# Kernel tuning notes

Hardware: AMD Instinct MI355X
Metric: run time of the kernel (lower is better)

Reference implementation:

```python
import jax, jax.numpy as jnp
import numpy as np

B, S, M, H, NH, FF = 8, 512, 512, 1024, 16, 4096
DH = H // NH      # 64
K = M + S         # key length = mem_len + sentence_len
EPS = 1e-5


def setup_inputs() -> dict:
    key = jax.random.key(0)
    ks = jax.random.split(key, 14)
    p = lambda k, shp: jax.random.normal(k, shp, jnp.float32) * 0.02
    return {
        "token_embedding": jax.random.normal(ks[0], (B, S, H), jnp.float32),
        "rel_pos_embedding": jax.random.normal(ks[1], (K, H), jnp.float32),
        "mems": jax.random.normal(ks[2], (B, M, H), jnp.float32),
        "segment_num": 1,
        "layer_num": 0,
        "Wq": p(ks[3], (H, H)), "Wk": p(ks[4], (H, H)), "Wv": p(ks[5], (H, H)),
        "Wr": p(ks[6], (H, H)), "Wo": p(ks[7], (H, H)),
        "u_bias": p(ks[8], (NH, DH)), "v_bias": p(ks[9], (NH, DH)),
        "gamma": jnp.ones((H,), jnp.float32), "beta": jnp.zeros((H,), jnp.float32),
        "W1": p(ks[10], (H, FF)), "b1": jnp.zeros((FF,), jnp.float32),
        "W2": p(ks[11], (FF, H)), "b2": jnp.zeros((H,), jnp.float32),
    }


def _rel_shift(x):
    # Transformer-XL relative shift. x: [B, NH, S, K]
    b, nh, s, k = x.shape
    x = jnp.pad(x, ((0, 0), (0, 0), (0, 0), (1, 0)))          # [B,NH,S,K+1]
    x = x.reshape(b, nh, k + 1, s)[:, :, 1:, :]               # drop first row
    return x.reshape(b, nh, s, k)


def _layer_norm(x, gamma, beta):
    mu = jnp.mean(x, axis=-1, keepdims=True)
    var = jnp.mean(jnp.square(x - mu), axis=-1, keepdims=True)
    return (x - mu) / jnp.sqrt(var + EPS) * gamma + beta


def reference(token_embedding, rel_pos_embedding, mems, segment_num, layer_num,
              Wq, Wk, Wv, Wr, Wo, u_bias, v_bias, gamma, beta, W1, b1, W2, b2):
    x = token_embedding                                   # [B,S,H]
    cat = jnp.concatenate([mems, x], axis=1)              # [B,K,H]
    q = (x @ Wq).reshape(B, S, NH, DH)
    k = (cat @ Wk).reshape(B, K, NH, DH)
    v = (cat @ Wv).reshape(B, K, NH, DH)
    r = (rel_pos_embedding @ Wr).reshape(K, NH, DH)
    # content + position terms (Transformer-XL)
    AC = jnp.einsum('bsnd,bknd->bnsk', q + u_bias, k)
    BD = _rel_shift(jnp.einsum('bsnd,knd->bnsk', q + v_bias, r))
    scores = (AC + BD) / jnp.sqrt(jnp.float32(DH))        # [B,NH,S,K]
    # causal mask with memory: query i sees keys j <= i + mem_len
    i = jnp.arange(S)[:, None]
    j = jnp.arange(K)[None, :]
    scores = jnp.where(j <= i + M, scores, jnp.float32(-1e9))
    attn = jax.nn.softmax(scores, axis=-1)
    ctx = jnp.einsum('bnsk,bknd->bsnd', attn, v).reshape(B, S, H)
    attn_out = ctx @ Wo
    # residual + LN
    h = _layer_norm(attn_out + x, gamma, beta)
    # FFN (relu), residual + LN (same LN params reused, as in source)
    ff = jax.nn.relu(h @ W1 + b1) @ W2 + b2
    y = _layer_norm(ff + h, gamma, beta)
    new_mems = jax.lax.stop_gradient(cat[:, -M:])
    return y, new_mems
```

## Files before the change

kernel.cpp:

```cpp
#include <hip/hip_runtime.h>


typedef float  floatx4 __attribute__((ext_vector_type(4)));
typedef __bf16 bf16x8  __attribute__((ext_vector_type(8)));

#define MFMA16(a, b, c) __builtin_amdgcn_mfma_f32_16x16x32_bf16((a), (b), (c), 0, 0, 0)
#define CFENCE() __asm__ __volatile__("" ::: "memory")

typedef __attribute__((address_space(1))) void gv_t;
typedef __attribute__((address_space(3))) void lv_t;

__device__ __forceinline__ void g2l16(const void* g, void* l) {
  __builtin_amdgcn_global_load_lds((gv_t*)g, (lv_t*)l, 16, 0, 0);
}

__device__ __forceinline__ floatx4 zf4() { floatx4 z = {0.f, 0.f, 0.f, 0.f}; return z; }

__device__ __forceinline__ bool in_is_bf16(const void* gamma_raw) {
  return *(const unsigned*)gamma_raw == 0x3F803F80u;
}

struct F8 { float v[8]; };

__device__ __forceinline__ F8 load8(const void* p, size_t i, bool bf) {
  F8 r;
  if (bf) {
    bf16x8 t = *(const bf16x8*)((const __bf16*)p + i);
#pragma unroll
    for (int j = 0; j < 8; j++) r.v[j] = (float)t[j];
  } else {
    floatx4 a = *(const floatx4*)((const float*)p + i);
    floatx4 b = *(const floatx4*)((const float*)p + i + 4);
#pragma unroll
    for (int j = 0; j < 4; j++) { r.v[j] = a[j]; r.v[4 + j] = b[j]; }
  }
  return r;
}

__device__ __forceinline__ void store8b(__bf16* p, size_t i, F8 r) {
  bf16x8 t;
#pragma unroll
  for (int j = 0; j < 8; j++) t[j] = (__bf16)r.v[j];
  *(bf16x8*)(p + i) = t;
}

__device__ __forceinline__ void store8raw(void* p, size_t i, F8 r, bool bf) {
  if (bf) {
    store8b((__bf16*)p, i, r);
  } else {
    floatx4 a, b;
#pragma unroll
    for (int j = 0; j < 4; j++) { a[j] = r.v[j]; b[j] = r.v[4 + j]; }
    *(floatx4*)((float*)p + i) = a;
    *(floatx4*)((float*)p + i + 4) = b;
  }
}

enum { EP_PLAIN = 0, EP_ADDRES = 2, EP_BIAS_RELU = 3, EP_BIAS_RES = 4 };

template <int MODE, int BM>
__global__ __launch_bounds__(256) void gemm_bt(
    const __bf16* __restrict__ A, const __bf16* __restrict__ Bt,
    __bf16* __restrict__ C, const float* __restrict__ bias1,
    const __bf16* __restrict__ res, int M, int N, int K) {
  constexpr int FR = BM / 32;
  __shared__ __attribute__((aligned(16))) __bf16 As[BM * 32];
  __shared__ __attribute__((aligned(16))) __bf16 Bs[128 * 32];
  const int t = threadIdx.x;
  const int lane = t & 63, w = t >> 6;
  const int l15 = lane & 15, quad = lane >> 4;
  const int row0 = blockIdx.y * BM, col0 = blockIdx.x * 128;

  floatx4 acc[FR][4];
#pragma unroll
  for (int i = 0; i < FR; i++)
#pragma unroll
    for (int j = 0; j < 4; j++) acc[i][j] = zf4();

  const int srow = 16 * w + (lane >> 2);
  const int soff = (lane & 3) * 8;
  const __bf16* gA0 = A + (size_t)(row0 + srow) * K + soff;
  const __bf16* gA1 = A + (size_t)(row0 + 64 + srow) * K + soff;
  const __bf16* gB0 = Bt + (size_t)(col0 + srow) * K + soff;
  const __bf16* gB1 = Bt + (size_t)(col0 + 64 + srow) * K + soff;
  __bf16* lA0 = As + srow * 32 + soff;
  __bf16* lA1 = As + (64 + srow) * 32 + soff;
  __bf16* lB0 = Bs + srow * 32 + soff;
  __bf16* lB1 = Bs + (64 + srow) * 32 + soff;

  const int wr = (w >> 1) * (BM / 2), wc = (w & 1) * 64;

  for (int kk = 0; kk < K; kk += 32) {
    g2l16(gA0 + kk, lA0);
    if constexpr (BM == 128) g2l16(gA1 + kk, lA1);
    g2l16(gB0 + kk, lB0);
    g2l16(gB1 + kk, lB1);
    __syncthreads();
    bf16x8 af[FR], bfr[4];
#pragma unroll
    for (int fr = 0; fr < FR; fr++)
      af[fr] = *(const bf16x8*)(As + (wr + fr * 16 + l15) * 32 + quad * 8);
#pragma unroll
    for (int fc = 0; fc < 4; fc++)
      bfr[fc] = *(const bf16x8*)(Bs + (wc + fc * 16 + l15) * 32 + quad * 8);
#pragma unroll
    for (int fr = 0; fr < FR; fr++)
#pragma unroll
      for (int fc = 0; fc < 4; fc++) acc[fr][fc] = MFMA16(af[fr], bfr[fc], acc[fr][fc]);
    __syncthreads();
  }

#pragma unroll
  for (int fr = 0; fr < FR; fr++) {
#pragma unroll
    for (int fc = 0; fc < 4; fc++) {
#pragma unroll
      for (int r = 0; r < 4; r++) {
        const int row = row0 + wr + fr * 16 + quad * 4 + r;
        const int col = col0 + wc + fc * 16 + l15;
        const size_t idx = (size_t)row * N + col;
        const float v = acc[fr][fc][r];
        if (MODE == EP_ADDRES) {
          C[idx] = (__bf16)(v + (float)res[idx]);
        } else if (MODE == EP_BIAS_RELU) {
          float u = v + bias1[col];
          C[idx] = (__bf16)(u > 0.f ? u : 0.f);
        } else if (MODE == EP_BIAS_RES) {
          C[idx] = (__bf16)(v + bias1[col] + (float)res[idx]);
        } else {
          C[idx] = (__bf16)v;
        }
      }
    }
  }
}

__global__ __launch_bounds__(256) void proj_gemm(
    const __bf16* __restrict__ xb, const __bf16* __restrict__ catb,
    const __bf16* __restrict__ relb, const __bf16* __restrict__ WqT,
    const __bf16* __restrict__ WkT, const __bf16* __restrict__ WvT,
    const __bf16* __restrict__ WrT, __bf16* __restrict__ qb,
    __bf16* __restrict__ kb, __bf16* __restrict__ vb, __bf16* __restrict__ rbo) {
  const int tid = (int)(blockIdx.x & 7) * 168 + (int)(blockIdx.x >> 3);
  const __bf16 *A, *Bt;
  __bf16* C;
  int local;
  if (tid < 256)       { A = xb;   Bt = WqT; C = qb;  local = tid; }
  else if (tid < 768)  { A = catb; Bt = WkT; C = kb;  local = tid - 256; }
  else if (tid < 1280) { A = catb; Bt = WvT; C = vb;  local = tid - 768; }
  else                 { A = relb; Bt = WrT; C = rbo; local = tid - 1280; }
  const int row0 = (local >> 3) * 128, col0 = (local & 7) * 128;

  __shared__ __attribute__((aligned(16))) __bf16 As[128 * 32];
  __shared__ __attribute__((aligned(16))) __bf16 Bs[128 * 32];
  const int t = threadIdx.x;
  const int lane = t & 63, w = t >> 6;
  const int l15 = lane & 15, quad = lane >> 4;

  floatx4 acc[4][4];
#pragma unroll
  for (int i = 0; i < 4; i++)
#pragma unroll
    for (int j = 0; j < 4; j++) acc[i][j] = zf4();

  const int srow = 16 * w + (lane >> 2);
  const int soff = (lane & 3) * 8;
  const __bf16* gA0 = A + (((size_t)(row0 + srow)) << 10) + soff;
  const __bf16* gA1 = A + (((size_t)(row0 + 64 + srow)) << 10) + soff;
  const __bf16* gB0 = Bt + (((size_t)(col0 + srow)) << 10) + soff;
  const __bf16* gB1 = Bt + (((size_t)(col0 + 64 + srow)) << 10) + soff;
  __bf16* lA0 = As + srow * 32 + soff;
  __bf16* lA1 = As + (64 + srow) * 32 + soff;
  __bf16* lB0 = Bs + srow * 32 + soff;
  __bf16* lB1 = Bs + (64 + srow) * 32 + soff;

  const int wr = (w >> 1) * 64, wc = (w & 1) * 64;

  for (int kk = 0; kk < 1024; kk += 32) {
    g2l16(gA0 + kk, lA0);
    g2l16(gA1 + kk, lA1);
    g2l16(gB0 + kk, lB0);
    g2l16(gB1 + kk, lB1);
    __syncthreads();
    bf16x8 af[4], bfr[4];
#pragma unroll
    for (int fr = 0; fr < 4; fr++)
      af[fr] = *(const bf16x8*)(As + (wr + fr * 16 + l15) * 32 + quad * 8);
#pragma unroll
    for (int fc = 0; fc < 4; fc++)
      bfr[fc] = *(const bf16x8*)(Bs + (wc + fc * 16 + l15) * 32 + quad * 8);
#pragma unroll
    for (int fr = 0; fr < 4; fr++)
#pragma unroll
      for (int fc = 0; fc < 4; fc++) acc[fr][fc] = MFMA16(af[fr], bfr[fc], acc[fr][fc]);
    __syncthreads();
  }

#pragma unroll
  for (int fr = 0; fr < 4; fr++) {
#pragma unroll
    for (int fc = 0; fc < 4; fc++) {
#pragma unroll
      for (int r = 0; r < 4; r++) {
        const int row = row0 + wr + fr * 16 + quad * 4 + r;
        const int col = col0 + wc + fc * 16 + l15;
        C[((size_t)row << 10) + col] = (__bf16)acc[fr][fc][r];
      }
    }
  }
}

__global__ __launch_bounds__(256, 4) void attn_kernel(
    const __bf16* __restrict__ qb, const __bf16* __restrict__ kb,
    const __bf16* __restrict__ vb, const __bf16* __restrict__ rb,
    const float* __restrict__ uf, const float* __restrict__ vf,
    __bf16* __restrict__ ctx) {
  __shared__ __attribute__((aligned(16))) __bf16 qL[64 * 72];
  __shared__ __attribute__((aligned(16))) __bf16 kL[64 * 72];
  __shared__ __attribute__((aligned(16))) __bf16 vtL[64 * 72];
  __shared__ __attribute__((aligned(16))) __bf16 pS[4 * 1152];

  const int t = threadIdx.x;
  const int lane = t & 63, w = t >> 6;
  const int l15 = lane & 15, quad = lane >> 4;
  const int i0 = (int)((blockIdx.x + blockIdx.z) & 7) * 64;
  const int n = blockIdx.y;
  const int b = blockIdx.z;

  {
    const int r = t >> 2, c = (t & 3) * 8;
    const size_t g = ((size_t)(b * 512 + i0 + r) << 10) + (n << 6) + c;
    *(bf16x8*)(qL + r * 72 + c) = *(const bf16x8*)(qb + g);
    *(bf16x8*)(qL + r * 72 + c + 32) = *(const bf16x8*)(qb + g + 32);
  }

  floatx4 o[4];
  float mrun[4], lrun[4];
#pragma unroll
  for (int i = 0; i < 4; i++) { o[i] = zf4(); mrun[i] = -1e30f; lrun[i] = 0.f; }

  bf16x8 aqu[2], aqv[2];
  __bf16* pp = pS + w * 1152;

  const int jmax = i0 + 512;
  for (int j0 = 0; j0 <= jmax; j0 += 64) {
    {
      const int r = t >> 2, c = (t & 3) * 8;
      const size_t g = ((size_t)(b * 1024 + j0 + r) << 10) + (n << 6) + c;
      *(bf16x8*)(kL + r * 72 + c) = *(const bf16x8*)(kb + g);
      *(bf16x8*)(kL + r * 72 + c + 32) = *(const bf16x8*)(kb + g + 32);
      bf16x8 v8a = *(const bf16x8*)(vb + g);
      bf16x8 v8b = *(const bf16x8*)(vb + g + 32);
      const int kb8 = ((((r >> 3) ^ ((c >> 3) << 1)) & 7) << 3) | (r & 7);
#pragma unroll
      for (int j = 0; j < 8; j++) {
        vtL[(c + j) * 72 + kb8] = v8a[j];
        vtL[(c + 32 + j) * 72 + kb8] = v8b[j];
      }
    }
    __syncthreads();

    if (j0 == 0) {
#pragma unroll
      for (int ks = 0; ks < 2; ks++) {
        bf16x8 qf = *(const bf16x8*)(qL + (16 * w + l15) * 72 + ks * 32 + quad * 8);
        const int dbase = (n << 6) + ks * 32 + quad * 8;
#pragma unroll
        for (int j = 0; j < 8; j++) {
          const float qv_ = (float)qf[j];
          aqu[ks][j] = (__bf16)(qv_ + uf[dbase + j]);
          aqv[ks][j] = (__bf16)(qv_ + vf[dbase + j]);
        }
      }
    }

    floatx4 s[4];
#pragma unroll
    for (int cf = 0; cf < 4; cf++) s[cf] = zf4();
#pragma unroll
    for (int ks = 0; ks < 2; ks++)
#pragma unroll
      for (int cf = 0; cf < 4; cf++) {
        bf16x8 bfr = *(const bf16x8*)(kL + (cf * 16 + l15) * 72 + ks * 32 + quad * 8);
        s[cf] = MFMA16(aqu[ks], bfr, s[cf]);
      }

    floatx4 bnd[5];
#pragma unroll
    for (int i = 0; i < 5; i++) bnd[i] = zf4();
    const int bw = j0 - i0 - 16 * w + 496;
#pragma unroll
    for (int ks = 0; ks < 2; ks++)
#pragma unroll
      for (int cf2 = 0; cf2 < 5; cf2++) {
        int rel = bw + cf2 * 16 + l15;
        rel = rel > 1023 ? 1023 : rel;
        bf16x8 bfr = *(const bf16x8*)(rb + ((size_t)rel << 10) + (n << 6) + ks * 32 + quad * 8);
        bnd[cf2] = MFMA16(aqv[ks], bfr, bnd[cf2]);
      }

    const bool mt = (j0 == jmax);
#pragma unroll
    for (int r = 0; r < 4; r++) {
      const int li = quad * 4 + r;
      const int tt = l15 + 15 - li;
      const int src = (quad << 4) | (tt & 15);
      float pm[5];
#pragma unroll
      for (int c5 = 0; c5 < 5; c5++) pm[c5] = __shfl(bnd[c5][r], src);
      const bool hi = (tt >> 4) != 0;
#pragma unroll
      for (int cf = 0; cf < 4; cf++) {
        const float bd = hi ? pm[cf + 1] : pm[cf];
        float sv = (s[cf][r] + bd) * 0.125f;
        if (mt && (cf * 16 + l15) > 16 * w + li) sv = -1e9f;
        s[cf][r] = sv;
      }
    }

    float alpha[4], mnew[4];
#pragma unroll
    for (int r = 0; r < 4; r++) {
      float mx = fmaxf(fmaxf(s[0][r], s[1][r]), fmaxf(s[2][r], s[3][r]));
#pragma unroll
      for (int d = 1; d < 16; d <<= 1) mx = fmaxf(mx, __shfl_xor(mx, d));
      mnew[r] = fmaxf(mrun[r], mx);
      alpha[r] = __expf(mrun[r] - mnew[r]);
      mrun[r] = mnew[r];
    }
#pragma unroll
    for (int cf = 0; cf < 4; cf++)
#pragma unroll
      for (int r = 0; r < 4; r++) s[cf][r] = __expf(s[cf][r] - mnew[r]);
#pragma unroll
    for (int r = 0; r < 4; r++) {
      float rs = s[0][r] + s[1][r] + s[2][r] + s[3][r];
#pragma unroll
      for (int d = 1; d < 16; d <<= 1) rs += __shfl_xor(rs, d);
      lrun[r] = lrun[r] * alpha[r] + rs;
    }
#pragma unroll
    for (int of = 0; of < 4; of++) {
      floatx4 ov = o[of];
#pragma unroll
      for (int r = 0; r < 4; r++) ov[r] *= alpha[r];
      o[of] = ov;
    }

#pragma unroll
    for (int cf = 0; cf < 4; cf++)
#pragma unroll
      for (int r = 0; r < 4; r++)
        pp[(quad * 4 + r) * 72 + cf * 16 + l15] = (__bf16)s[cf][r];
    CFENCE();
#pragma unroll
    for (int ks = 0; ks < 2; ks++) {
      bf16x8 pa = *(const bf16x8*)(pp + l15 * 72 + ks * 32 + quad * 8);
#pragma unroll
      for (int of = 0; of < 4; of++) {
        const int row = of * 16 + l15;
        const int kbx = (ks * 4 + quad) ^ (((row >> 3) & 3) << 1);
        bf16x8 bv = *(const bf16x8*)(vtL + row * 72 + kbx * 8);
        o[of] = MFMA16(pa, bv, o[of]);
      }
    }
    __syncthreads();
  }

#pragma unroll
  for (int r = 0; r < 4; r++) {
    const float inv = 1.f / lrun[r];
    const int row = i0 + 16 * w + quad * 4 + r;
#pragma unroll
    for (int of = 0; of < 4; of++)
      ctx[((size_t)(b * 512 + row) << 10) + (n << 6) + of * 16 + l15] =
          (__bf16)(o[of][r] * inv);
  }
}

template <int RAW>
__global__ __launch_bounds__(256) void ln_kernel(
    const __bf16* __restrict__ in, const float* __restrict__ gf,
    const float* __restrict__ bf_, __bf16* __restrict__ outb,
    void* __restrict__ outraw, const void* __restrict__ gamma_raw) {
  const int t = threadIdx.x;
  const int lane = t & 63, w = t >> 6;
  const size_t row = (size_t)blockIdx.x * 4 + w;
  const __bf16* p = in + (row << 10) + lane * 16;
  bf16x8 v0 = *(const bf16x8*)(p);
  bf16x8 v1 = *(const bf16x8*)(p + 8);
  float f[16];
#pragma unroll
  for (int j = 0; j < 8; j++) { f[j] = (float)v0[j]; f[8 + j] = (float)v1[j]; }
  float s = 0.f, ss = 0.f;
#pragma unroll
  for (int j = 0; j < 16; j++) { s += f[j]; ss += f[j] * f[j]; }
#pragma unroll
  for (int d = 1; d < 64; d <<= 1) { s += __shfl_xor(s, d); ss += __shfl_xor(ss, d); }
  const float mu = s * (1.f / 1024.f);
  const float var = ss * (1.f / 1024.f) - mu * mu;
  const float rstd = rsqrtf(var + 1e-5f);
  float gv[16], bv[16];
#pragma unroll
  for (int j = 0; j < 16; j += 4) {
    floatx4 g = *(const floatx4*)(gf + lane * 16 + j);
    floatx4 bb = *(const floatx4*)(bf_ + lane * 16 + j);
#pragma unroll
    for (int q = 0; q < 4; q++) { gv[j + q] = g[q]; bv[j + q] = bb[q]; }
  }
  float r[16];
#pragma unroll
  for (int j = 0; j < 16; j++) r[j] = (f[j] - mu) * rstd * gv[j] + bv[j];

  if (RAW == 0) {
    bf16x8 o0, o1;
#pragma unroll
    for (int j = 0; j < 8; j++) { o0[j] = (__bf16)r[j]; o1[j] = (__bf16)r[8 + j]; }
    *(bf16x8*)(outb + (row << 10) + lane * 16) = o0;
    *(bf16x8*)(outb + (row << 10) + lane * 16 + 8) = o1;
  } else {
    const bool bf = in_is_bf16(gamma_raw);
    if (bf) {
      __bf16* o = (__bf16*)outraw;
      bf16x8 o0, o1;
#pragma unroll
      for (int j = 0; j < 8; j++) { o0[j] = (__bf16)r[j]; o1[j] = (__bf16)r[8 + j]; }
      *(bf16x8*)(o + (row << 10) + lane * 16) = o0;
      *(bf16x8*)(o + (row << 10) + lane * 16 + 8) = o1;
    } else {
      float* o = (float*)outraw + (row << 10) + lane * 16;
#pragma unroll
      for (int j = 0; j < 16; j += 4) {
        floatx4 q;
#pragma unroll
        for (int k = 0; k < 4; k++) q[k] = r[j + k];
        *(floatx4*)(o + j) = q;
      }
    }
  }
}

__global__ __launch_bounds__(256) void prep_kernel(
    const void* __restrict__ x, const void* __restrict__ mems,
    const void* __restrict__ relp, const void* __restrict__ gamma_raw,
    __bf16* __restrict__ catb, __bf16* __restrict__ xb,
    __bf16* __restrict__ relb, void* __restrict__ dout) {
  const bool bf = in_is_bf16(gamma_raw);
  const size_t idx = (size_t)blockIdx.x * 256 + threadIdx.x;
  if (idx < 1048576) {
    const size_t e = idx * 8;
    const int rowk = (int)(e >> 10);
    const int col = (int)(e & 1023);
    const int b = rowk >> 10, pos = rowk & 1023;
    F8 v = (pos < 512)
               ? load8(mems, (((size_t)(b * 512 + pos)) << 10) + col, bf)
               : load8(x, (((size_t)(b * 512 + pos - 512)) << 10) + col, bf);
    store8b(catb, e, v);
  } else if (idx < 1572864) {
    const size_t e = (idx - 1048576) * 8;
    store8b(xb, e, load8(x, e, bf));
  } else if (idx < 1703936) {
    const size_t e = (idx - 1572864) * 8;
    store8b(relb, e, load8(relp, e, bf));
  } else {
    const size_t e = (idx - 1703936) * 8;
    store8raw(dout, (size_t)4194304 + e, load8(x, e, bf), bf);
  }
}

__global__ __launch_bounds__(256) void bias_conv_kernel(
    const void* ub, const void* vb, const void* b1, const void* b2,
    const void* gamma, const void* beta, const void* gamma_raw,
    float* __restrict__ dst) {
  const bool bf = in_is_bf16(gamma_raw);
  const int j = blockIdx.x * 256 + threadIdx.x;
  const void* src;
  int k;
  if (j < 1024)        { src = ub;    k = j; }
  else if (j < 2048)   { src = vb;    k = j - 1024; }
  else if (j < 6144)   { src = b1;    k = j - 2048; }
  else if (j < 7168)   { src = b2;    k = j - 6144; }
  else if (j < 8192)   { src = gamma; k = j - 7168; }
  else if (j < 9216)   { src = beta;  k = j - 8192; }
  else return;
  dst[j] = bf ? (float)((const __bf16*)src)[k] : ((const float*)src)[k];
}

__device__ __forceinline__ void transpose_tile(
    const void* __restrict__ W, __bf16* __restrict__ Wt, int K, int N,
    int k0, int n0, bool bf, __bf16* tile) {
  const int t = threadIdx.x;
  const int r = t >> 2, c = (t & 3) * 8;
  F8 a = load8(W, (size_t)(k0 + r) * N + n0 + c, bf);
  F8 b = load8(W, (size_t)(k0 + r) * N + n0 + c + 32, bf);
  bf16x8 ta, tb;
#pragma unroll
  for (int j = 0; j < 8; j++) { ta[j] = (__bf16)a.v[j]; tb[j] = (__bf16)b.v[j]; }
  *(bf16x8*)(tile + r * 72 + c) = ta;
  *(bf16x8*)(tile + r * 72 + c + 32) = tb;
  __syncthreads();
  bf16x8 o0, o1;
#pragma unroll
  for (int j = 0; j < 8; j++) {
    o0[j] = tile[(c + j) * 72 + r];
    o1[j] = tile[(c + 32 + j) * 72 + r];
  }
  *(bf16x8*)(Wt + (size_t)(n0 + r) * K + k0 + c) = o0;
  *(bf16x8*)(Wt + (size_t)(n0 + r) * K + k0 + c + 32) = o1;
}

__global__ __launch_bounds__(256) void qkvro_transpose_kernel(
    const void* __restrict__ Wq, const void* __restrict__ Wk,
    const void* __restrict__ Wv, const void* __restrict__ Wr,
    const void* __restrict__ Wo, const void* __restrict__ gamma_raw,
    __bf16* __restrict__ WqT, __bf16* __restrict__ WkT,
    __bf16* __restrict__ WvT, __bf16* __restrict__ WrT,
    __bf16* __restrict__ WoT) {
  __shared__ __attribute__((aligned(16))) __bf16 tile[64 * 72];
  const bool bf = in_is_bf16(gamma_raw);
  const void* W;
  __bf16* Wt;
  switch (blockIdx.z) {
    case 0: W = Wq; Wt = WqT; break;
    case 1: W = Wk; Wt = WkT; break;
    case 2: W = Wv; Wt = WvT; break;
    case 3: W = Wr; Wt = WrT; break;
    default: W = Wo; Wt = WoT; break;
  }
  transpose_tile(W, Wt, 1024, 1024, blockIdx.y * 64, blockIdx.x * 64, bf, tile);
}

__global__ __launch_bounds__(256) void big_transpose_kernel(
    const void* __restrict__ W1, const void* __restrict__ W2,
    const void* __restrict__ gamma_raw, __bf16* __restrict__ W1T,
    __bf16* __restrict__ W2T) {
  __shared__ __attribute__((aligned(16))) __bf16 tile[64 * 72];
  const bool bf = in_is_bf16(gamma_raw);
  const int bx = blockIdx.x, by = blockIdx.y;
  if (blockIdx.z == 0) {
    transpose_tile(W1, W1T, 1024, 4096, by * 64, bx * 64, bf, tile);
  } else {
    transpose_tile(W2, W2T, 4096, 1024, (by * 4 + (bx >> 4)) * 64, (bx & 15) * 64,
                   bf, tile);
  }
}

extern "C" void kernel_launch(void* const* d_in, const int* in_sizes, int n_in,
                              void* d_out, int out_size, void* d_ws, size_t ws_size,
                              hipStream_t stream) {
  const void* x = d_in[0];
  const void* relp = d_in[1];
  const void* mems = d_in[2];
  const void* Wq = d_in[5];
  const void* Wk = d_in[6];
  const void* Wv = d_in[7];
  const void* Wr = d_in[8];
  const void* Wo = d_in[9];
  const void* ub = d_in[10];
  const void* vbias = d_in[11];
  const void* gamma = d_in[12];
  const void* beta = d_in[13];
  const void* W1 = d_in[14];
  const void* b1 = d_in[15];
  const void* W2 = d_in[16];
  const void* b2 = d_in[17];

  char* ws = (char*)d_ws;
  const size_t MB = (size_t)1 << 20;
  __bf16* catb = (__bf16*)(ws);
  __bf16* ctx  = (__bf16*)(ws);
  __bf16* ff1  = (__bf16*)(ws);
  __bf16* kb   = (__bf16*)(ws + 16 * MB);
  __bf16* vb   = (__bf16*)(ws + 32 * MB);
  __bf16* ao   = (__bf16*)(ws + 32 * MB);
  __bf16* hb   = (__bf16*)(ws + 40 * MB);
  __bf16* qb   = (__bf16*)(ws + 48 * MB);
  __bf16* ff2  = (__bf16*)(ws + 48 * MB);
  __bf16* xb   = (__bf16*)(ws + 56 * MB);
  __bf16* W1T  = (__bf16*)(ws + 56 * MB);
  __bf16* relb = (__bf16*)(ws + 64 * MB);
  __bf16* rb   = (__bf16*)(ws + 66 * MB);
  __bf16* WqT  = (__bf16*)(ws + 68 * MB);
  __bf16* WkT  = (__bf16*)(ws + 70 * MB);
  __bf16* W2T  = (__bf16*)(ws + 64 * MB);
  __bf16* WvT  = (__bf16*)(ws + 72 * MB);
  __bf16* WrT  = (__bf16*)(ws + 74 * MB);
  __bf16* WoT  = (__bf16*)(ws + 76 * MB);
  float*  uf   = (float*)(ws + 78 * MB);
  float*  vf   = uf + 1024;
  float*  b1f  = uf + 2048;
  float*  b2f  = uf + 6144;
  float*  gf   = uf + 7168;
  float*  betf = uf + 8192;

  prep_kernel<<<dim3(8704), 256, 0, stream>>>(x, mems, relp, gamma, catb, xb, relb, d_out);
  bias_conv_kernel<<<dim3(36), 256, 0, stream>>>(ub, vbias, b1, b2, gamma, beta, gamma, uf);
  qkvro_transpose_kernel<<<dim3(16, 16, 5), 256, 0, stream>>>(
      Wq, Wk, Wv, Wr, Wo, gamma, WqT, WkT, WvT, WrT, WoT);

  proj_gemm<<<dim3(1344), 256, 0, stream>>>(xb, catb, relb, WqT, WkT, WvT, WrT,
                                            qb, kb, vb, rb);

  attn_kernel<<<dim3(8, 16, 8), 256, 0, stream>>>(qb, kb, vb, rb, uf, vf, ctx);

  gemm_bt<EP_ADDRES, 64><<<dim3(8, 64), 256, 0, stream>>>(ctx, WoT, ao, nullptr, xb,
                                                          4096, 1024, 1024);
  ln_kernel<0><<<dim3(1024), 256, 0, stream>>>(ao, gf, betf, hb, nullptr, nullptr);

  big_transpose_kernel<<<dim3(64, 16, 2), 256, 0, stream>>>(W1, W2, gamma, W1T, W2T);

  gemm_bt<EP_BIAS_RELU, 128><<<dim3(32, 32), 256, 0, stream>>>(hb, W1T, ff1, b1f,
                                                               nullptr, 4096, 4096, 1024);
  gemm_bt<EP_BIAS_RES, 64><<<dim3(8, 64), 256, 0, stream>>>(ff1, W2T, ff2, b2f, hb,
                                                            4096, 1024, 4096);
  ln_kernel<1><<<dim3(1024), 256, 0, stream>>>(ff2, gf, betf, nullptr, d_out, gamma);

  (void)in_sizes; (void)n_in; (void)out_size; (void)ws_size;
}
```

Before: 514.6 us.

## Write V transposed from projection GEMM and use DPP row reductions in attention

The V projection epilogue now writes V in a head-major transposed layout, so the attention kernel loads V^T rows with vector loads and stores them straight into swizzled LDS instead of doing per-element scatter transposes. Softmax row max and sum reductions across 16 lanes now use DPP moves instead of __shfl_xor, which avoids the LDS-backed permute path. In exchange the V epilogue does strided 8-byte global stores, and the swizzle must match the existing vtL read pattern.

After: 513.5 us. Within noise of the previous version (-0.2%).

```diff
diff --git a/kernel.cpp b/kernel.cpp
--- a/kernel.cpp
+++ b/kernel.cpp
@@ -3,6 +3,7 @@
 
 typedef float  floatx4 __attribute__((ext_vector_type(4)));
 typedef __bf16 bf16x8  __attribute__((ext_vector_type(8)));
+typedef __bf16 bf16x4  __attribute__((ext_vector_type(4)));
 
 #define MFMA16(a, b, c) __builtin_amdgcn_mfma_f32_16x16x32_bf16((a), (b), (c), 0, 0, 0)
 #define CFENCE() __asm__ __volatile__("" ::: "memory")
@@ -15,6 +16,26 @@
 }
 
 __device__ __forceinline__ floatx4 zf4() { floatx4 z = {0.f, 0.f, 0.f, 0.f}; return z; }
+
+template <int CTRL>
+__device__ __forceinline__ float dppf(float v) {
+  return __builtin_bit_cast(
+      float, __builtin_amdgcn_mov_dpp(__builtin_bit_cast(int, v), CTRL, 0xF, 0xF, true));
+}
+__device__ __forceinline__ float red16_max(float x) {
+  x = fmaxf(x, dppf<0xB1>(x));
+  x = fmaxf(x, dppf<0x4E>(x));
+  x = fmaxf(x, dppf<0x124>(x));
+  x = fmaxf(x, dppf<0x128>(x));
+  return x;
+}
+__device__ __forceinline__ float red16_sum(float x) {
+  x += dppf<0xB1>(x);
+  x += dppf<0x4E>(x);
+  x += dppf<0x124>(x);
+  x += dppf<0x128>(x);
+  return x;
+}
 
 __device__ __forceinline__ bool in_is_bf16(const void* gamma_raw) {
   return *(const unsigned*)gamma_raw == 0x3F803F80u;
@@ -140,14 +161,15 @@
     const __bf16* __restrict__ relb, const __bf16* __restrict__ WqT,
     const __bf16* __restrict__ WkT, const __bf16* __restrict__ WvT,
     const __bf16* __restrict__ WrT, __bf16* __restrict__ qb,
-    __bf16* __restrict__ kb, __bf16* __restrict__ vb, __bf16* __restrict__ rbo) {
+    __bf16* __restrict__ kb, __bf16* __restrict__ vtb, __bf16* __restrict__ rbo) {
   const int tid = (int)(blockIdx.x & 7) * 168 + (int)(blockIdx.x >> 3);
   const __bf16 *A, *Bt;
   __bf16* C;
   int local;
+  bool isV = false;
   if (tid < 256)       { A = xb;   Bt = WqT; C = qb;  local = tid; }
   else if (tid < 768)  { A = catb; Bt = WkT; C = kb;  local = tid - 256; }
-  else if (tid < 1280) { A = catb; Bt = WvT; C = vb;  local = tid - 768; }
+  else if (tid < 1280) { A = catb; Bt = WvT; C = vtb; local = tid - 768; isV = true; }
   else                 { A = relb; Bt = WrT; C = rbo; local = tid - 1280; }
   const int row0 = (local >> 3) * 128, col0 = (local & 7) * 128;
 
@@ -196,15 +218,32 @@
     __syncthreads();
   }
 
-#pragma unroll
-  for (int fr = 0; fr < 4; fr++) {
-#pragma unroll
-    for (int fc = 0; fc < 4; fc++) {
-#pragma unroll
-      for (int r = 0; r < 4; r++) {
-        const int row = row0 + wr + fr * 16 + quad * 4 + r;
+  if (isV) {
+#pragma unroll
+    for (int fr = 0; fr < 4; fr++) {
+      const int row = row0 + wr + fr * 16 + quad * 4;
+      const int b_ = row >> 10;
+      const int pos = row & 1023;
+#pragma unroll
+      for (int fc = 0; fc < 4; fc++) {
         const int col = col0 + wc + fc * 16 + l15;
-        C[((size_t)row << 10) + col] = (__bf16)acc[fr][fc][r];
+        bf16x4 pk;
+#pragma unroll
+        for (int r = 0; r < 4; r++) pk[r] = (__bf16)acc[fr][fc][r];
+        *(bf16x4*)(C + (((size_t)(b_ * 1024 + col)) << 10) + pos) = pk;
+      }
+    }
+  } else {
+#pragma unroll
+    for (int fr = 0; fr < 4; fr++) {
+#pragma unroll
+      for (int fc = 0; fc < 4; fc++) {
+#pragma unroll
+        for (int r = 0; r < 4; r++) {
+          const int row = row0 + wr + fr * 16 + quad * 4 + r;
+          const int col = col0 + wc + fc * 16 + l15;
+          C[((size_t)row << 10) + col] = (__bf16)acc[fr][fc][r];
+        }
       }
     }
   }
@@ -212,7 +251,7 @@
 
 __global__ __launch_bounds__(256, 4) void attn_kernel(
     const __bf16* __restrict__ qb, const __bf16* __restrict__ kb,
-    const __bf16* __restrict__ vb, const __bf16* __restrict__ rb,
+    const __bf16* __restrict__ vtb, const __bf16* __restrict__ rb,
     const float* __restrict__ uf, const float* __restrict__ vf,
     __bf16* __restrict__ ctx) {
   __shared__ __attribute__((aligned(16))) __bf16 qL[64 * 72];
@@ -246,17 +285,15 @@
   for (int j0 = 0; j0 <= jmax; j0 += 64) {
     {
       const int r = t >> 2, c = (t & 3) * 8;
-      const size_t g = ((size_t)(b * 1024 + j0 + r) << 10) + (n << 6) + c;
-      *(bf16x8*)(kL + r * 72 + c) = *(const bf16x8*)(kb + g);
-      *(bf16x8*)(kL + r * 72 + c + 32) = *(const bf16x8*)(kb + g + 32);
-      bf16x8 v8a = *(const bf16x8*)(vb + g);
-      bf16x8 v8b = *(const bf16x8*)(vb + g + 32);
-      const int kb8 = ((((r >> 3) ^ ((c >> 3) << 1)) & 7) << 3) | (r & 7);
-#pragma unroll
-      for (int j = 0; j < 8; j++) {
-        vtL[(c + j) * 72 + kb8] = v8a[j];
-        vtL[(c + 32 + j) * 72 + kb8] = v8b[j];
-      }
+      const size_t gk = ((size_t)(b * 1024 + j0 + r) << 10) + (n << 6) + c;
+      *(bf16x8*)(kL + r * 72 + c) = *(const bf16x8*)(kb + gk);
+      *(bf16x8*)(kL + r * 72 + c + 32) = *(const bf16x8*)(kb + gk + 32);
+      const size_t gv = ((size_t)((b * 16 + n) * 64 + r) << 10) + j0 + c;
+      bf16x8 v8a = *(const bf16x8*)(vtb + gv);
+      bf16x8 v8b = *(const bf16x8*)(vtb + gv + 32);
+      const int sw = ((r >> 3) & 3) << 1;
+      *(bf16x8*)(vtL + r * 72 + (((c >> 3) ^ sw) << 3)) = v8a;
+      *(bf16x8*)(vtL + r * 72 + ((((c >> 3) + 4) ^ sw) << 3)) = v8b;
     }
     __syncthreads();
 
@@ -322,8 +359,7 @@
 #pragma unroll
     for (int r = 0; r < 4; r++) {
       float mx = fmaxf(fmaxf(s[0][r], s[1][r]), fmaxf(s[2][r], s[3][r]));
-#pragma unroll
-      for (int d = 1; d < 16; d <<= 1) mx = fmaxf(mx, __shfl_xor(mx, d));
+      mx = red16_max(mx);
       mnew[r] = fmaxf(mrun[r], mx);
       alpha[r] = __expf(mrun[r] - mnew[r]);
       mrun[r] = mnew[r];
@@ -335,8 +371,7 @@
 #pragma unroll
     for (int r = 0; r < 4; r++) {
       float rs = s[0][r] + s[1][r] + s[2][r] + s[3][r];
-#pragma unroll
-      for (int d = 1; d < 16; d <<= 1) rs += __shfl_xor(rs, d);
+      rs = red16_sum(rs);
       lrun[r] = lrun[r] * alpha[r] + rs;
     }
 #pragma unroll
@@ -571,7 +606,7 @@
   __bf16* ctx  = (__bf16*)(ws);
   __bf16* ff1  = (__bf16*)(ws);
   __bf16* kb   = (__bf16*)(ws + 16 * MB);
-  __bf16* vb   = (__bf16*)(ws + 32 * MB);
+  __bf16* vtb  = (__bf16*)(ws + 32 * MB);
   __bf16* ao   = (__bf16*)(ws + 32 * MB);
   __bf16* hb   = (__bf16*)(ws + 40 * MB);
   __bf16* qb   = (__bf16*)(ws + 48 * MB);
@@ -599,9 +634,9 @@
       Wq, Wk, Wv, Wr, Wo, gamma, WqT, WkT, WvT, WrT, WoT);
 
   proj_gemm<<<dim3(1344), 256, 0, stream>>>(xb, catb, relb, WqT, WkT, WvT, WrT,
-                                            qb, kb, vb, rb);
-
-  attn_kernel<<<dim3(8, 16, 8), 256, 0, stream>>>(qb, kb, vb, rb, uf, vf, ctx);
+                                            qb, kb, vtb, rb);
+
+  attn_kernel<<<dim3(8, 16, 8), 256, 0, stream>>>(qb, kb, vtb, rb, uf, vf, ctx);
 
   gemm_bt<EP_ADDRES, 64><<<dim3(8, 64), 256, 0, stream>>>(ctx, WoT, ao, nullptr, xb,
                                                           4096, 1024, 1024);
```
